# Performance work log

Hardware: AMD Instinct MI355X
Metric: run time of the kernel (lower is better)

The kernel has to match this reference:

```python
import jax, jax.numpy as jnp
import numpy as np

B, T, D, H, DH = 2, 1024, 1024, 16, 64
DFF, V = 4096, 32000
L0, NLAT, WIN = 512, 4, 3
R, ALPHA = 8, 16
LATENT_ID = 31999


def _ln(x, s, b):
    m = x.mean(-1, keepdims=True)
    v = ((x - m) ** 2).mean(-1, keepdims=True)
    return (x - m) * jax.lax.rsqrt(v + 1e-5) * s + b


def _lm(embeds, Wpos, Wqkv, bqkv, Aq, Bq, Wo, bo, Ao, Bo, W1, b1, W2, b2,
        ln1_s, ln1_b, ln2_s, ln2_b, lnf_s, lnf_b):
    # single pre-LN transformer block with LoRA-merged c_attn/c_proj + final LN
    S = embeds.shape[1]
    sc = ALPHA / R
    h = embeds + Wpos[:S]
    a = _ln(h, ln1_s, ln1_b)
    qkv = a @ (Wqkv + sc * (Aq @ Bq)) + bqkv          # [B,S,3D]
    q, k, v = [t.reshape(B, S, H, DH) for t in jnp.split(qkv, 3, axis=-1)]
    scores = jnp.einsum('bqhd,bkhd->bhqk', q, k) / 8.0  # sqrt(DH)=8
    mask = jnp.tril(jnp.ones((S, S), bool))
    attn = jax.nn.softmax(jnp.where(mask, scores, -1e9), axis=-1)
    ctx = jnp.einsum('bhqk,bkhd->bqhd', attn, v).reshape(B, S, D)
    h = h + ctx @ (Wo + sc * (Ao @ Bo)) + bo
    m = _ln(h, ln2_s, ln2_b)
    h = h + jax.nn.gelu(m @ W1 + b1) @ W2 + b2
    return _ln(h, lnf_s, lnf_b)


def setup_inputs() -> dict:
    key = jax.random.key(0)
    ks = jax.random.split(key, 16)
    init = lambda k, shape, scale: jax.random.normal(k, shape, jnp.float32) * scale
    input_ids = jax.random.randint(ks[0], (B, T), 0, V)
    input_ids = input_ids.at[:, L0:L0 + NLAT].set(LATENT_ID)  # latent slots
    return {
        'input_ids': input_ids.astype(jnp.int32),
        'attention_mask': jnp.ones((B, T), jnp.int32),
        'labels': jax.random.randint(ks[1], (B, T), 0, V).astype(jnp.int32),
        'position_ids': jnp.broadcast_to(jnp.arange(T, dtype=jnp.int32), (B, T)),
        'embed': init(ks[2], (V, D), 0.02),
        'Wpos': init(ks[3], (T, D), 0.01),
        'Wqkv': init(ks[4], (D, 3 * D), 0.02), 'bqkv': jnp.zeros((3 * D,)),
        'Aq': init(ks[5], (D, R), 0.02), 'Bq': init(ks[6], (R, 3 * D), 0.02),
        'Wo': init(ks[7], (D, D), 0.02), 'bo': jnp.zeros((D,)),
        'Ao': init(ks[8], (D, R), 0.02), 'Bo': init(ks[9], (R, D), 0.02),
        'W1': init(ks[10], (D, DFF), 0.02), 'b1': jnp.zeros((DFF,)),
        'W2': init(ks[11], (DFF, D), 0.02), 'b2': jnp.zeros((D,)),
        'ln1_s': jnp.ones((D,)), 'ln1_b': jnp.zeros((D,)),
        'ln2_s': jnp.ones((D,)), 'ln2_b': jnp.zeros((D,)),
        'lnf_s': jnp.ones((D,)), 'lnf_b': jnp.zeros((D,)),
        'latent_w': jnp.zeros((WIN,)),
    }


def reference(input_ids, attention_mask, labels, position_ids, embed, Wpos,
              Wqkv, bqkv, Aq, Bq, Wo, bo, Ao, Bo, W1, b1, W2, b2,
              ln1_s, ln1_b, ln2_s, ln2_b, lnf_s, lnf_b, latent_w):
    lm = lambda e: _lm(e, Wpos, Wqkv, bqkv, Aq, Bq, Wo, bo, Ao, Bo,
                       W1, b1, W2, b2, ln1_s, ln1_b, ln2_s, ln2_b, lnf_s, lnf_b)
    embeds = embed[input_ids]                     # [B,T,D]
    parts = []
    for p in range(NLAT):                         # fixed small iterative-pass count
        start = 0 if p == 0 else L0 + p - 1       # segment processed this pass
        end = L0 + p
        hid = lm(embeds[:, :end])                 # frozen-prefix recompute == kv cache
        parts.append(hid[:, start:end] @ embed.T) # segment logits (tied lm_head)
        tok = L0 + p                              # latent slot filled this pass
        n = min(WIN, tok - start)                 # window clipped to segment offset
        w = jax.nn.softmax(latent_w[WIN - n:])    # softmax over last n weights
        vec = jnp.einsum('w,bwd->bd', w, hid[:, tok - n:tok])
        embeds = embeds.at[:, tok].set(vec)       # scatter into latent slot
    hid = lm(embeds)
    parts.append(hid[:, L0 + NLAT - 1:] @ embed.T)
    logits = jnp.concatenate(parts, axis=1)       # [B,T,V]
    logp = jax.nn.log_softmax(logits[:, :-1], axis=-1)
    nll = -jnp.take_along_axis(logp, labels[:, 1:, None].astype(jnp.int32), axis=-1)
    return nll.mean()
```

## Files before the change

kernel.cpp:

```cpp
#include <hip/hip_runtime.h>
#include <math.h>

#define B_   2
#define T_   1024
#define D_   1024
#define H_   16
#define DH_  64
#define DFF_ 4096
#define V_   32000
#define NTOK 2046
#define NCH  250

typedef __attribute__((ext_vector_type(8))) short short8;
typedef __attribute__((ext_vector_type(4))) float floatx4;

__device__ __forceinline__ unsigned short f2bf(float x) {
    unsigned int u = __float_as_uint(x);
    unsigned int r = (u + 0x7fffu + ((u >> 16) & 1u)) >> 16;
    return (unsigned short)r;
}

__device__ __forceinline__ float bf2f(unsigned short u) {
    return __uint_as_float((unsigned int)u << 16);
}

__device__ __forceinline__ void gld_lds16(void* lds, const void* g) {
    __builtin_amdgcn_global_load_lds(
        (const __attribute__((address_space(1))) void*)g,
        (__attribute__((address_space(3))) void*)lds, 16, 0, 0);
}

__device__ __forceinline__ float gelu_tanh(float x) {
    float x3 = x * x * x;
    return 0.5f * x * (1.0f + tanhf(0.7978845608028654f * (x + 0.044715f * x3)));
}

__global__ __launch_bounds__(256) void k_prep_w(const float* __restrict__ W,
        const float* __restrict__ A, const float* __restrict__ Bm,
        unsigned short* __restrict__ out, int K, int N, int lora) {
    __shared__ float t[64][65];
    int n0 = blockIdx.x * 64, k0 = blockIdx.y * 64;
    int tid = threadIdx.x;
    int nn = tid & 63, kb = tid >> 6;
    for (int i = 0; i < 16; i++) {
        int kk = kb * 16 + i;
        float v = W[(size_t)(k0 + kk) * N + n0 + nn];
        if (lora) {
            float s = 0.f;
#pragma unroll
            for (int r = 0; r < 8; r++) s += A[(k0 + kk) * 8 + r] * Bm[r * N + n0 + nn];
            v += 2.0f * s;
        }
        t[kk][nn] = v;
    }
    __syncthreads();
    int kk2 = tid & 63, nb = tid >> 6;
    for (int j = 0; j < 16; j++) {
        int nn2 = nb * 16 + j;
        out[(size_t)(n0 + nn2) * K + k0 + kk2] = f2bf(t[kk2][nn2]);
    }
}

__global__ void k_f2bf(const float* __restrict__ in, unsigned short* __restrict__ out, int n4) {
    int i = blockIdx.x * 256 + threadIdx.x;
    if (i >= n4) return;
    float4 v = ((const float4*)in)[i];
    ushort4 o;
    o.x = f2bf(v.x); o.y = f2bf(v.y); o.z = f2bf(v.z); o.w = f2bf(v.w);
    ((ushort4*)out)[i] = o;
}

__global__ void k_embed_gather(const int* __restrict__ ids, const float* __restrict__ embed,
                               float* __restrict__ embeds) {
    int bt = blockIdx.x;
    int d4 = threadIdx.x;
    int id = ids[bt];
    ((float4*)embeds)[(size_t)bt * 256 + d4] = ((const float4*)embed)[(size_t)id * 256 + d4];
}

__global__ __launch_bounds__(256) void k_ln(const float* __restrict__ in,
                                            const float* __restrict__ embeds, const float* __restrict__ Wpos,
                                            const float* __restrict__ sc, const float* __restrict__ bi,
                                            float* __restrict__ hout, float* __restrict__ outf,
                                            unsigned short* __restrict__ outbf,
                                            int c0, int range, int strided_bf) {
    int r = blockIdx.x;
    int b = r / range, pos = c0 + r % range;
    size_t rowoff = (size_t)(b * T_ + pos) * D_;
    int tid = threadIdx.x;
    float xv[4];
    if (embeds) {
#pragma unroll
        for (int j = 0; j < 4; j++) {
            int i = tid + j * 256;
            xv[j] = embeds[rowoff + i] + Wpos[(size_t)pos * D_ + i];
            hout[rowoff + i] = xv[j];
        }
    } else {
#pragma unroll
        for (int j = 0; j < 4; j++) xv[j] = in[rowoff + tid + j * 256];
    }
    float s1 = 0.f, s2 = 0.f;
#pragma unroll
    for (int j = 0; j < 4; j++) { s1 += xv[j]; s2 += xv[j] * xv[j]; }
    __shared__ float r1[256], r2[256];
    r1[tid] = s1; r2[tid] = s2; __syncthreads();
    for (int o = 128; o > 0; o >>= 1) {
        if (tid < o) { r1[tid] += r1[tid + o]; r2[tid] += r2[tid + o]; }
        __syncthreads();
    }
    float mean = r1[0] * (1.0f / D_);
    float var = r2[0] * (1.0f / D_) - mean * mean;
    float inv = rsqrtf(var + 1e-5f);
    size_t bfrow = strided_bf ? (size_t)(b * T_ + pos) : (size_t)r;
#pragma unroll
    for (int j = 0; j < 4; j++) {
        int i = tid + j * 256;
        float y = (xv[j] - mean) * inv * sc[i] + bi[i];
        if (outf) outf[rowoff + i] = y;
        outbf[bfrow * D_ + i] = f2bf(y);
    }
}

template <int MODE>
__global__ __launch_bounds__(256) void k_mgemm(const unsigned short* __restrict__ Abf,
        const unsigned short* __restrict__ Bt, const float* __restrict__ bias,
        float* __restrict__ o0, unsigned short* __restrict__ u0,
        unsigned short* __restrict__ u1, unsigned short* __restrict__ u2,
        int M, int N, int K, int c0, int range, int ksegs) {
    __shared__ short8 As_v[256];
    __shared__ short8 Bs_v[512];
    int tid = threadIdx.x;
    int lane = tid & 63, w = tid >> 6;
    int quad = lane >> 4, l15 = lane & 15;
    int row0 = blockIdx.y * 64, col0 = blockIdx.x * 128;
    int kseg = blockIdx.z;
    int Klen = K / ksegs;
    int ksoff = kseg * Klen;
    int wr = w >> 1, wc = w & 1;

    int arow = row0 + lane; if (arow >= M) arow = M - 1;
    const unsigned short* ga  = Abf + (size_t)arow * K + ksoff + w * 8;
    int bcol = col0 + (w & 1) * 64 + lane;
    const unsigned short* gb1 = Bt + (size_t)bcol * K + ksoff + (w >> 1) * 8;
    const unsigned short* gb2 = Bt + (size_t)bcol * K + ksoff + (2 + (w >> 1)) * 8;

    floatx4 acc[2][4];
#pragma unroll
    for (int i = 0; i < 2; i++)
#pragma unroll
        for (int j = 0; j < 4; j++)
#pragma unroll
            for (int k = 0; k < 4; k++) acc[i][j][k] = 0.f;

    int iters = Klen >> 5;
    for (int it = 0; it < iters; ++it) {
        __syncthreads();
        gld_lds16(&As_v[w * 64],        ga);
        gld_lds16(&Bs_v[w * 64],        gb1);
        gld_lds16(&Bs_v[256 + w * 64],  gb2);
        ga += 32; gb1 += 32; gb2 += 32;
        __syncthreads();
        short8 af[2], bfv[4];
#pragma unroll
        for (int mi = 0; mi < 2; mi++) af[mi] = As_v[quad * 64 + wr * 32 + mi * 16 + l15];
#pragma unroll
        for (int nj = 0; nj < 4; nj++) bfv[nj] = Bs_v[quad * 128 + wc * 64 + nj * 16 + l15];
#pragma unroll
        for (int mi = 0; mi < 2; mi++)
#pragma unroll
            for (int nj = 0; nj < 4; nj++)
                acc[mi][nj] = __builtin_amdgcn_mfma_f32_16x16x32_bf16(af[mi], bfv[nj], acc[mi][nj], 0, 0, 0);
    }

#pragma unroll
    for (int mi = 0; mi < 2; mi++)
#pragma unroll
        for (int reg = 0; reg < 4; reg++) {
            int r = row0 + wr * 32 + mi * 16 + quad * 4 + reg;
            if (r >= M) continue;
            int b = r / range, pos = c0 + r % range;
#pragma unroll
            for (int nj = 0; nj < 4; nj++) {
                int n = col0 + wc * 64 + nj * 16 + l15;
                if constexpr (MODE == 1) {
                    float v = acc[mi][nj][reg] + bias[n];
                    if (n < 1024) u0[(size_t)r * 1024 + n] = f2bf(v);
                    else if (n < 2048) u1[(size_t)(b * T_ + pos) * 1024 + (n - 1024)] = f2bf(v);
                    else u2[(size_t)(b * T_ + pos) * 1024 + (n - 2048)] = f2bf(v);
                } else if constexpr (MODE == 2) {
                    float v = acc[mi][nj][reg] + (kseg == 0 ? bias[n] : 0.f);
                    atomicAdd(&o0[(size_t)(b * T_ + pos) * D_ + n], v);
                } else if constexpr (MODE == 3) {
                    float v = acc[mi][nj][reg] + bias[n];
                    u0[(size_t)r * N + n] = f2bf(gelu_tanh(v));
                }
            }
        }
}

template <int MODE>
__global__ __launch_bounds__(256) void k_sgemm(const unsigned short* __restrict__ Abf,
        const unsigned short* __restrict__ Bt, const float* __restrict__ bias,
        float* __restrict__ o0, unsigned short* __restrict__ u0,
        unsigned short* __restrict__ u1, unsigned short* __restrict__ u2,
        int N, int K, int c0) {
    __shared__ unsigned short lds_a[2 * 4096];
    __shared__ float lds_p[4][64][2];
    int tid = threadIdx.x, lane = tid & 63, w = tid >> 6;
    int n = blockIdx.x * 64 + lane;
    int nv = (2 * K) >> 3;
    for (int v = tid; v < nv; v += 256)
        *(short8*)&lds_a[v * 8] = *(const short8*)&Abf[v * 8];
    __syncthreads();
    int kq = K >> 2;
    int k0 = w * kq;
    float a0 = 0.f, a1 = 0.f;
    const unsigned short* bp = Bt + (size_t)n * K + k0;
    for (int i = 0; i < kq; i += 8) {
        short8 bv  = *(const short8*)(bp + i);
        short8 av0 = *(const short8*)&lds_a[k0 + i];
        short8 av1 = *(const short8*)&lds_a[K + k0 + i];
#pragma unroll
        for (int j = 0; j < 8; j++) {
            float bf_ = bf2f((unsigned short)bv[j]);
            a0 += bf2f((unsigned short)av0[j]) * bf_;
            a1 += bf2f((unsigned short)av1[j]) * bf_;
        }
    }
    lds_p[w][lane][0] = a0;
    lds_p[w][lane][1] = a1;
    __syncthreads();
    if (tid < 128) {
        int l = tid & 63, m = tid >> 6;
        int nn = blockIdx.x * 64 + l;
        float acc = lds_p[0][l][m] + lds_p[1][l][m] + lds_p[2][l][m] + lds_p[3][l][m];
        int b = m, pos = c0;
        if constexpr (MODE == 4) {
            float v = acc + bias[nn];
            if (nn < 1024) u0[(size_t)m * 1024 + nn] = f2bf(v);
            else if (nn < 2048) u1[(size_t)(b * T_ + pos) * 1024 + (nn - 1024)] = f2bf(v);
            else {
                int idx = nn - 2048, h = idx >> 6, d = idx & 63;
                u2[(size_t)((b * 16 + h) * 64 + d) * T_ + pos] = f2bf(v);
            }
        } else if constexpr (MODE == 2) {
            o0[(size_t)(b * T_ + pos) * D_ + nn] += acc + bias[nn];
        } else if constexpr (MODE == 3) {
            u0[(size_t)m * N + nn] = f2bf(gelu_tanh(acc + bias[nn]));
        }
    }
}

__global__ __launch_bounds__(256) void k_vtrans(const unsigned short* __restrict__ vcbf,
        unsigned short* __restrict__ vtc, int c0, int range) {
    __shared__ unsigned short ts[64][72];
    int pt = blockIdx.x, h = blockIdx.y, b = blockIdx.z;
    int t = threadIdx.x;
#pragma unroll
    for (int i = 0; i < 2; i++) {
        int idx = t + i * 256;
        int p = idx >> 3, c8 = idx & 7;
        int pos = c0 + pt * 64 + p;
        if (pos < c0 + range) {
            short8 v = *(const short8*)&vcbf[(size_t)(b * T_ + pos) * D_ + h * 64 + c8 * 8];
            *(short8*)&ts[p][c8 * 8] = v;
        }
    }
    __syncthreads();
#pragma unroll
    for (int i = 0; i < 2; i++) {
        int idx = t + i * 256;
        int d = idx >> 3, p8 = idx & 7;
        unsigned short tmp[8];
#pragma unroll
        for (int j = 0; j < 8; j++) tmp[j] = ts[p8 * 8 + j][d];
        int pos0 = c0 + pt * 64 + p8 * 8;
        size_t rb = (size_t)((b * 16 + h) * 64 + d) * T_;
        if (pos0 + 7 < c0 + range) {
            *(short8*)&vtc[rb + pos0] = *(short8*)tmp;
        } else {
            for (int j = 0; j < 8; j++)
                if (pos0 + j < c0 + range) vtc[rb + pos0 + j] = tmp[j];
        }
    }
}

__global__ __launch_bounds__(256) void k_fattn(const unsigned short* __restrict__ qbf,
        const unsigned short* __restrict__ kcbf, const unsigned short* __restrict__ vtc,
        unsigned short* __restrict__ ctxbf, int c0, int range) {
    __shared__ unsigned short pw[4][16][72];
    int tid = threadIdx.x;
    int w = tid >> 6, lane = tid & 63, quad = lane >> 4, l15 = lane & 15;
    int qt = blockIdx.x, h = blockIdx.y, b = blockIdx.z;
    int q0 = qt * 64 + w * 16;
    if (q0 >= range) return;
    int qtop = q0 + 15; if (qtop >= range) qtop = range - 1;
    int nkt = (c0 + qtop) / 64 + 1;

    int qrow = q0 + l15; if (qrow >= range) qrow = range - 1;
    const unsigned short* qp = qbf + (size_t)(b * range + qrow) * D_ + h * 64 + quad * 8;
    short8 aq0 = *(const short8*)qp;
    short8 aq1 = *(const short8*)(qp + 32);

    floatx4 oacc[4];
#pragma unroll
    for (int dg = 0; dg < 4; dg++)
#pragma unroll
        for (int r = 0; r < 4; r++) oacc[dg][r] = 0.f;
    float m_r[4] = {-1e30f, -1e30f, -1e30f, -1e30f};
    float l_r[4] = {0.f, 0.f, 0.f, 0.f};

    const unsigned short* kb_p = kcbf + (size_t)b * T_ * D_ + h * 64 + quad * 8;
    const unsigned short* vb_p = vtc + (size_t)((b * 16 + h) * 64 + l15) * T_ + quad * 8;

    for (int kt = 0; kt < nkt; kt++) {
        int kb = kt * 64;
        floatx4 s[4];
#pragma unroll
        for (int g = 0; g < 4; g++) {
            const unsigned short* kp = kb_p + (size_t)(kb + g * 16 + l15) * D_;
            short8 bk0 = *(const short8*)kp;
            short8 bk1 = *(const short8*)(kp + 32);
            floatx4 z; z[0] = 0.f; z[1] = 0.f; z[2] = 0.f; z[3] = 0.f;
            z = __builtin_amdgcn_mfma_f32_16x16x32_bf16(aq0, bk0, z, 0, 0, 0);
            s[g] = __builtin_amdgcn_mfma_f32_16x16x32_bf16(aq1, bk1, z, 0, 0, 0);
        }
#pragma unroll
        for (int r = 0; r < 4; r++) {
            int qpos = c0 + q0 + quad * 4 + r;
            float mx = -1e30f;
#pragma unroll
            for (int g = 0; g < 4; g++) {
                int kpos = kb + g * 16 + l15;
                float sv = (kpos <= qpos) ? s[g][r] * 0.125f : -1e30f;
                s[g][r] = sv; mx = fmaxf(mx, sv);
            }
            mx = fmaxf(mx, __shfl_xor(mx, 1));
            mx = fmaxf(mx, __shfl_xor(mx, 2));
            mx = fmaxf(mx, __shfl_xor(mx, 4));
            mx = fmaxf(mx, __shfl_xor(mx, 8));
            float mn = fmaxf(m_r[r], mx);
            float alpha = __expf(m_r[r] - mn);
            m_r[r] = mn;
            float ls = 0.f;
#pragma unroll
            for (int g = 0; g < 4; g++) {
                float p = __expf(s[g][r] - mn);
                s[g][r] = p; ls += p;
            }
            ls += __shfl_xor(ls, 1);
            ls += __shfl_xor(ls, 2);
            ls += __shfl_xor(ls, 4);
            ls += __shfl_xor(ls, 8);
            l_r[r] = l_r[r] * alpha + ls;
#pragma unroll
            for (int dg = 0; dg < 4; dg++) oacc[dg][r] *= alpha;
        }
#pragma unroll
        for (int g = 0; g < 4; g++)
#pragma unroll
            for (int r = 0; r < 4; r++)
                pw[w][quad * 4 + r][g * 16 + l15] = f2bf(s[g][r]);
        short8 ap0 = *(const short8*)&pw[w][l15][quad * 8];
        short8 ap1 = *(const short8*)&pw[w][l15][32 + quad * 8];
#pragma unroll
        for (int dg = 0; dg < 4; dg++) {
            const unsigned short* vp = vb_p + (size_t)(dg * 16) * T_ + kb;
            short8 bv0 = *(const short8*)vp;
            short8 bv1 = *(const short8*)(vp + 32);
            oacc[dg] = __builtin_amdgcn_mfma_f32_16x16x32_bf16(ap0, bv0, oacc[dg], 0, 0, 0);
            oacc[dg] = __builtin_amdgcn_mfma_f32_16x16x32_bf16(ap1, bv1, oacc[dg], 0, 0, 0);
        }
    }
#pragma unroll
    for (int dg = 0; dg < 4; dg++)
#pragma unroll
        for (int r = 0; r < 4; r++) {
            int qloc = q0 + quad * 4 + r;
            if (qloc < range)
                ctxbf[(size_t)(b * range + qloc) * D_ + h * 64 + dg * 16 + l15] =
                    f2bf(oacc[dg][r] / l_r[r]);
        }
}

__global__ void k_latent0(const float* __restrict__ hid, const float* __restrict__ lw,
                          float* __restrict__ embeds) {
    int idx = blockIdx.x * 256 + threadIdx.x;
    if (idx >= B_ * D_) return;
    int b = idx / D_, d = idx % D_;
    float w0 = lw[0], w1 = lw[1], w2 = lw[2];
    float mx = fmaxf(w0, fmaxf(w1, w2));
    float e0 = __expf(w0 - mx), e1 = __expf(w1 - mx), e2 = __expf(w2 - mx);
    float inv = 1.0f / (e0 + e1 + e2);
    float v = (e0 * hid[(size_t)(b * T_ + 509) * D_ + d] +
               e1 * hid[(size_t)(b * T_ + 510) * D_ + d] +
               e2 * hid[(size_t)(b * T_ + 511) * D_ + d]) * inv;
    embeds[(size_t)(b * T_ + 512) * D_ + d] = v;
}

__global__ void k_latent1(const float* __restrict__ hid, float* __restrict__ embeds, int tok) {
    int idx = blockIdx.x * 256 + threadIdx.x;
    if (idx >= B_ * D_) return;
    int b = idx / D_, d = idx % D_;
    embeds[(size_t)(b * T_ + tok) * D_ + d] = hid[(size_t)(b * T_ + tok - 1) * D_ + d];
}

__global__ __launch_bounds__(256) void k_loss1m(const unsigned short* __restrict__ hidbf,
        const unsigned short* __restrict__ embedbf, const int* __restrict__ labels,
        float* __restrict__ partm, float* __restrict__ parts, float* __restrict__ llogit) {
    __shared__ short8 As0[512], Bs0[512];
    __shared__ short8 As1[512], Bs1[512];
    __shared__ int lds_lab[128];
    __shared__ float lds_pm[128][2];
    __shared__ float lds_ps[128][2];
    int tid = threadIdx.x;
    int lane = tid & 63, w = tid >> 6;
    int quad = lane >> 4, l15 = lane & 15;
    int chunk = blockIdx.y;
    int row0 = blockIdx.x * 128, v0 = chunk * 128;
    int rh = (w >> 1) * 64, ch = (w & 1) * 64;

    if (tid < 128) {
        int tok = row0 + tid;
        lds_lab[tid] = (tok < NTOK) ? labels[tok + 1 + (tok >= 1023)] : -1;
    }

    int cA0 = w * 128 + lane, cA1 = cA0 + 64;
    int rA0 = cA0 & 127, kgA0 = cA0 >> 7;
    int rA1 = cA1 & 127, kgA1 = cA1 >> 7;
    int tokA0 = row0 + rA0; if (tokA0 >= NTOK) tokA0 = NTOK - 1;
    int tokA1 = row0 + rA1; if (tokA1 >= NTOK) tokA1 = NTOK - 1;
    const unsigned short* ga0 = hidbf + (size_t)(tokA0 + (tokA0 >= 1023)) * D_ + kgA0 * 8;
    const unsigned short* ga1 = hidbf + (size_t)(tokA1 + (tokA1 >= 1023)) * D_ + kgA1 * 8;
    const unsigned short* gb0 = embedbf + (size_t)(v0 + rA0) * D_ + kgA0 * 8;
    const unsigned short* gb1 = embedbf + (size_t)(v0 + rA1) * D_ + kgA1 * 8;

    floatx4 acc[4][4];
#pragma unroll
    for (int i = 0; i < 4; i++)
#pragma unroll
        for (int j = 0; j < 4; j++)
#pragma unroll
            for (int k = 0; k < 4; k++) acc[i][j][k] = 0.f;

#define LSTAGE(AS, BS) \
    gld_lds16(&AS[w * 128],      ga0); \
    gld_lds16(&AS[w * 128 + 64], ga1); \
    gld_lds16(&BS[w * 128],      gb0); \
    gld_lds16(&BS[w * 128 + 64], gb1); \
    ga0 += 32; ga1 += 32; gb0 += 32; gb1 += 32;

#define LCOMP(AS, BS) { \
    short8 af[4], bfv[4]; \
    _Pragma("unroll") \
    for (int mi = 0; mi < 4; mi++) af[mi] = AS[quad * 128 + rh + mi * 16 + l15]; \
    _Pragma("unroll") \
    for (int nj = 0; nj < 4; nj++) bfv[nj] = BS[quad * 128 + ch + nj * 16 + l15]; \
    _Pragma("unroll") \
    for (int mi = 0; mi < 4; mi++) \
        _Pragma("unroll") \
        for (int nj = 0; nj < 4; nj++) \
            acc[mi][nj] = __builtin_amdgcn_mfma_f32_16x16x32_bf16(af[mi], bfv[nj], acc[mi][nj], 0, 0, 0); }

#define WAIT_VM4_BAR \
    asm volatile("s_waitcnt vmcnt(4)" ::: "memory"); \
    __builtin_amdgcn_s_barrier(); \
    __builtin_amdgcn_sched_barrier(0);

#define WAIT_LGKM_BAR \
    asm volatile("s_waitcnt lgkmcnt(0)" ::: "memory"); \
    __builtin_amdgcn_s_barrier(); \
    __builtin_amdgcn_sched_barrier(0);

    LSTAGE(As0, Bs0)
    for (int itp = 0; itp < 15; ++itp) {
        LSTAGE(As1, Bs1)
        WAIT_VM4_BAR
        LCOMP(As0, Bs0)
        WAIT_LGKM_BAR
        LSTAGE(As0, Bs0)
        WAIT_VM4_BAR
        LCOMP(As1, Bs1)
        WAIT_LGKM_BAR
    }
    LSTAGE(As1, Bs1)
    WAIT_VM4_BAR
    LCOMP(As0, Bs0)
    WAIT_LGKM_BAR
    asm volatile("s_waitcnt vmcnt(0)" ::: "memory");
    __builtin_amdgcn_s_barrier();
    __builtin_amdgcn_sched_barrier(0);
    LCOMP(As1, Bs1)

#undef LSTAGE
#undef LCOMP
#undef WAIT_VM4_BAR
#undef WAIT_LGKM_BAR

#pragma unroll
    for (int mi = 0; mi < 4; mi++)
#pragma unroll
        for (int reg = 0; reg < 4; reg++) {
            int rloc = rh + mi * 16 + quad * 4 + reg;
            int lab = lds_lab[rloc];
            float vm = -1e30f;
#pragma unroll
            for (int nj = 0; nj < 4; nj++) {
                float v = acc[mi][nj][reg];
                int vcol = v0 + ch + nj * 16 + l15;
                if (vcol == lab) llogit[row0 + rloc] = v;
                vm = fmaxf(vm, v);
            }
            for (int off = 1; off < 16; off <<= 1) vm = fmaxf(vm, __shfl_xor(vm, off));
            float ss = 0.f;
#pragma unroll
            for (int nj = 0; nj < 4; nj++) ss += __expf(acc[mi][nj][reg] - vm);
            for (int off = 1; off < 16; off <<= 1) ss += __shfl_xor(ss, off);
            if (l15 == 0) { lds_pm[rloc][ch >> 6] = vm; lds_ps[rloc][ch >> 6] = ss; }
        }
    __syncthreads();
    if (tid < 128) {
        int tok = row0 + tid;
        if (tok < NTOK) {
            float m0 = lds_pm[tid][0], m1 = lds_pm[tid][1];
            float M = fmaxf(m0, m1);
            float S = lds_ps[tid][0] * __expf(m0 - M) + lds_ps[tid][1] * __expf(m1 - M);
            partm[(size_t)chunk * NTOK + tok] = M;
            parts[(size_t)chunk * NTOK + tok] = S;
        }
    }
}

__global__ void k_loss2a(const float* __restrict__ partm, const float* __restrict__ parts,
                         const float* __restrict__ ll, float* __restrict__ nll) {
    int tok = blockIdx.x * 256 + threadIdx.x;
    if (tok >= NTOK) return;
    float M = -1e30f;
    for (int c = 0; c < NCH; c++) M = fmaxf(M, partm[(size_t)c * NTOK + tok]);
    float S = 0.f;
    for (int c = 0; c < NCH; c++)
        S += parts[(size_t)c * NTOK + tok] * __expf(partm[(size_t)c * NTOK + tok] - M);
    nll[tok] = logf(S) + M - ll[tok];
}

__global__ __launch_bounds__(256) void k_loss2b(const float* __restrict__ nll, float* __restrict__ out) {
    __shared__ float red[256];
    int tid = threadIdx.x;
    float s = 0.f;
    for (int i = tid; i < NTOK; i += 256) s += nll[i];
    red[tid] = s; __syncthreads();
    for (int o = 128; o > 0; o >>= 1) {
        if (tid < o) red[tid] += red[tid + o];
        __syncthreads();
    }
    if (tid == 0) out[0] = red[0] / (float)NTOK;
}

extern "C" void kernel_launch(void* const* d_in, const int* in_sizes, int n_in,
                              void* d_out, int out_size, void* d_ws, size_t ws_size,
                              hipStream_t stream) {
    const int*   input_ids = (const int*)d_in[0];
    const int*   labels    = (const int*)d_in[2];
    const float* embed     = (const float*)d_in[4];
    const float* Wpos      = (const float*)d_in[5];
    const float* Wqkv      = (const float*)d_in[6];
    const float* bqkv      = (const float*)d_in[7];
    const float* Aq        = (const float*)d_in[8];
    const float* Bq        = (const float*)d_in[9];
    const float* Wo        = (const float*)d_in[10];
    const float* bo        = (const float*)d_in[11];
    const float* Ao        = (const float*)d_in[12];
    const float* Bo        = (const float*)d_in[13];
    const float* W1        = (const float*)d_in[14];
    const float* b1        = (const float*)d_in[15];
    const float* W2        = (const float*)d_in[16];
    const float* b2        = (const float*)d_in[17];
    const float* ln1_s     = (const float*)d_in[18];
    const float* ln1_b     = (const float*)d_in[19];
    const float* ln2_s     = (const float*)d_in[20];
    const float* ln2_b     = (const float*)d_in[21];
    const float* lnf_s     = (const float*)d_in[22];
    const float* lnf_b     = (const float*)d_in[23];
    const float* latent_w  = (const float*)d_in[24];

    char* base = (char*)d_ws;
    size_t off = 0;
    auto alloc = [&](size_t bytes) { void* p = base + off; off += (bytes + 255) & ~255ULL; return p; };

    float* embeds  = (float*)alloc((size_t)B_ * T_ * D_ * 4);
    float* hbuf    = (float*)alloc((size_t)B_ * T_ * D_ * 4);
    float* hidbuf  = (float*)alloc((size_t)B_ * T_ * D_ * 4);
    float* partm   = (float*)alloc((size_t)NCH * NTOK * 4);
    float* parts_  = (float*)alloc((size_t)NCH * NTOK * 4);
    float* llogit  = (float*)alloc((size_t)NTOK * 4);
    float* nllbuf  = (float*)alloc((size_t)NTOK * 4);
    unsigned short* wqkvT  = (unsigned short*)alloc((size_t)3072 * 1024 * 2);
    unsigned short* woT    = (unsigned short*)alloc((size_t)1024 * 1024 * 2);
    unsigned short* W1T    = (unsigned short*)alloc((size_t)4096 * 1024 * 2);
    unsigned short* W2T    = (unsigned short*)alloc((size_t)1024 * 4096 * 2);
    unsigned short* embedbf = (unsigned short*)alloc((size_t)V_ * D_ * 2);
    unsigned short* hidbf  = (unsigned short*)alloc((size_t)B_ * T_ * D_ * 2);
    unsigned short* abf    = (unsigned short*)alloc((size_t)1024 * D_ * 2);
    unsigned short* ctxbf  = (unsigned short*)alloc((size_t)1024 * D_ * 2);
    unsigned short* ffbw   = (unsigned short*)alloc((size_t)1024 * DFF_ * 2);
    unsigned short* qbf    = (unsigned short*)alloc((size_t)1024 * D_ * 2);
    unsigned short* kcbf   = (unsigned short*)alloc((size_t)B_ * T_ * D_ * 2);
    unsigned short* vcbf   = (unsigned short*)alloc((size_t)B_ * T_ * D_ * 2);
    unsigned short* vtc    = (unsigned short*)alloc((size_t)B_ * H_ * DH_ * T_ * 2);

    k_prep_w<<<dim3(3072 / 64, 1024 / 64), 256, 0, stream>>>(Wqkv, Aq, Bq, wqkvT, 1024, 3072, 1);
    k_prep_w<<<dim3(1024 / 64, 1024 / 64), 256, 0, stream>>>(Wo, Ao, Bo, woT, 1024, 1024, 1);
    k_prep_w<<<dim3(4096 / 64, 1024 / 64), 256, 0, stream>>>(W1, nullptr, nullptr, W1T, 1024, 4096, 0);
    k_prep_w<<<dim3(1024 / 64, 4096 / 64), 256, 0, stream>>>(W2, nullptr, nullptr, W2T, 4096, 1024, 0);
    k_f2bf<<<(V_ * D_ / 4 + 255) / 256, 256, 0, stream>>>(embed, embedbf, V_ * D_ / 4);
    k_embed_gather<<<B_ * T_, 256, 0, stream>>>(input_ids, embed, embeds);

    auto run_pass = [&](int c0, int c1) {
        int range = c1 - c0;
        int Mr = B_ * range;
        int gy = (Mr + 63) / 64;
        int qt = (range + 63) / 64;
        k_ln<<<Mr, 256, 0, stream>>>(nullptr, embeds, Wpos, ln1_s, ln1_b, hbuf, nullptr, abf, c0, range, 0);
        if (range == 1) {
            k_sgemm<4><<<3072 / 64, 256, 0, stream>>>(abf, wqkvT, bqkv, nullptr, qbf, kcbf, vtc,
                                                      3072, 1024, c0);
            k_fattn<<<dim3(1, H_, B_), 256, 0, stream>>>(qbf, kcbf, vtc, ctxbf, c0, 1);
            k_sgemm<2><<<1024 / 64, 256, 0, stream>>>(ctxbf, woT, bo, hbuf, nullptr, nullptr, nullptr,
                                                      1024, 1024, c0);
            k_ln<<<Mr, 256, 0, stream>>>(hbuf, nullptr, nullptr, ln2_s, ln2_b, nullptr, nullptr, abf, c0, range, 0);
            k_sgemm<3><<<4096 / 64, 256, 0, stream>>>(abf, W1T, b1, nullptr, ffbw, nullptr, nullptr,
                                                      4096, 1024, c0);
            k_sgemm<2><<<1024 / 64, 256, 0, stream>>>(ffbw, W2T, b2, hbuf, nullptr, nullptr, nullptr,
                                                      1024, 4096, c0);
        } else {
            k_mgemm<1><<<dim3(3072 / 128, gy), 256, 0, stream>>>(abf, wqkvT, bqkv, nullptr, qbf, kcbf, vcbf,
                                                                 Mr, 3072, 1024, c0, range, 1);
            k_vtrans<<<dim3(qt, H_, B_), 256, 0, stream>>>(vcbf, vtc, c0, range);
            k_fattn<<<dim3(qt, H_, B_), 256, 0, stream>>>(qbf, kcbf, vtc, ctxbf, c0, range);
            k_mgemm<2><<<dim3(1024 / 128, gy, 4), 256, 0, stream>>>(ctxbf, woT, bo, hbuf, nullptr, nullptr, nullptr,
                                                                    Mr, 1024, 1024, c0, range, 4);
            k_ln<<<Mr, 256, 0, stream>>>(hbuf, nullptr, nullptr, ln2_s, ln2_b, nullptr, nullptr, abf, c0, range, 0);
            k_mgemm<3><<<dim3(4096 / 128, gy), 256, 0, stream>>>(abf, W1T, b1, nullptr, ffbw, nullptr, nullptr,
                                                                 Mr, 4096, 1024, c0, range, 1);
            k_mgemm<2><<<dim3(1024 / 128, gy, 4), 256, 0, stream>>>(ffbw, W2T, b2, hbuf, nullptr, nullptr, nullptr,
                                                                    Mr, 1024, 4096, c0, range, 4);
        }
        k_ln<<<Mr, 256, 0, stream>>>(hbuf, nullptr, nullptr, lnf_s, lnf_b, nullptr, hidbuf, hidbf, c0, range, 1);
    };

    run_pass(0, 512);
    k_latent0<<<(B_ * D_ + 255) / 256, 256, 0, stream>>>(hidbuf, latent_w, embeds);
    run_pass(512, 513);
    k_latent1<<<(B_ * D_ + 255) / 256, 256, 0, stream>>>(hidbuf, embeds, 513);
    run_pass(513, 514);
    k_latent1<<<(B_ * D_ + 255) / 256, 256, 0, stream>>>(hidbuf, embeds, 514);
    run_pass(514, 515);
    k_latent1<<<(B_ * D_ + 255) / 256, 256, 0, stream>>>(hidbuf, embeds, 515);
    run_pass(515, 1024);

    k_loss1m<<<dim3((NTOK + 127) / 128, NCH), 256, 0, stream>>>(hidbf, embedbf, labels, partm, parts_, llogit);
    k_loss2a<<<(NTOK + 255) / 256, 256, 0, stream>>>(partm, parts_, llogit, nllbuf);
    k_loss2b<<<1, 256, 0, stream>>>(nllbuf, (float*)d_out);
}
```

Measured before the change: 1.264 ms.

## Double-buffer MFMA GEMM LDS loads and split-K the single-token GEMV kernels

The tiled MFMA GEMM now keeps two LDS buffers and issues the next K-tile's global-to-LDS loads before computing the current tile, using vmcnt waits and raw barriers so load latency overlaps the MFMA work. The single-row (range==1) GEMV path is split along K into more blocks, with partial sums either written to a scratch buffer and reduced by a finish kernel or accumulated with atomics, to use more CUs. This costs double the LDS per block, extra kernel launches and atomics, and the pipelined loop assumes an even number of K iterations.

```diff
diff --git a/kernel.cpp b/kernel.cpp
--- a/kernel.cpp
+++ b/kernel.cpp
@@ -128,8 +128,8 @@
         float* __restrict__ o0, unsigned short* __restrict__ u0,
         unsigned short* __restrict__ u1, unsigned short* __restrict__ u2,
         int M, int N, int K, int c0, int range, int ksegs) {
-    __shared__ short8 As_v[256];
-    __shared__ short8 Bs_v[512];
+    __shared__ short8 As0[256], Bs0[512];
+    __shared__ short8 As1[256], Bs1[512];
     int tid = threadIdx.x;
     int lane = tid & 63, w = tid >> 6;
     int quad = lane >> 4, l15 = lane & 15;
@@ -154,24 +154,50 @@
             for (int k = 0; k < 4; k++) acc[i][j][k] = 0.f;
 
     int iters = Klen >> 5;
-    for (int it = 0; it < iters; ++it) {
-        __syncthreads();
-        gld_lds16(&As_v[w * 64],        ga);
-        gld_lds16(&Bs_v[w * 64],        gb1);
-        gld_lds16(&Bs_v[256 + w * 64],  gb2);
-        ga += 32; gb1 += 32; gb2 += 32;
-        __syncthreads();
-        short8 af[2], bfv[4];
-#pragma unroll
-        for (int mi = 0; mi < 2; mi++) af[mi] = As_v[quad * 64 + wr * 32 + mi * 16 + l15];
-#pragma unroll
-        for (int nj = 0; nj < 4; nj++) bfv[nj] = Bs_v[quad * 128 + wc * 64 + nj * 16 + l15];
-#pragma unroll
-        for (int mi = 0; mi < 2; mi++)
-#pragma unroll
-            for (int nj = 0; nj < 4; nj++)
-                acc[mi][nj] = __builtin_amdgcn_mfma_f32_16x16x32_bf16(af[mi], bfv[nj], acc[mi][nj], 0, 0, 0);
-    }
+
+#define MSTAGE(AS, BS) \
+    gld_lds16(&AS[w * 64],       ga); \
+    gld_lds16(&BS[w * 64],       gb1); \
+    gld_lds16(&BS[256 + w * 64], gb2); \
+    ga += 32; gb1 += 32; gb2 += 32;
+
+#define MCOMP(AS, BS) { \
+    short8 af[2], bfv[4]; \
+    _Pragma("unroll") \
+    for (int mi = 0; mi < 2; mi++) af[mi] = AS[quad * 64 + wr * 32 + mi * 16 + l15]; \
+    _Pragma("unroll") \
+    for (int nj = 0; nj < 4; nj++) bfv[nj] = BS[quad * 128 + wc * 64 + nj * 16 + l15]; \
+    _Pragma("unroll") \
+    for (int mi = 0; mi < 2; mi++) \
+        _Pragma("unroll") \
+        for (int nj = 0; nj < 4; nj++) \
+            acc[mi][nj] = __builtin_amdgcn_mfma_f32_16x16x32_bf16(af[mi], bfv[nj], acc[mi][nj], 0, 0, 0); }
+
+#define MWVM3 \
+    asm volatile("s_waitcnt vmcnt(3)" ::: "memory"); \
+    __builtin_amdgcn_s_barrier(); \
+    __builtin_amdgcn_sched_barrier(0);
+
+#define MWLG \
+    asm volatile("s_waitcnt lgkmcnt(0)" ::: "memory"); \
+    __builtin_amdgcn_s_barrier(); \
+    __builtin_amdgcn_sched_barrier(0);
+
+    MSTAGE(As0, Bs0)
+    for (int itp = 0; itp < (iters >> 1) - 1; ++itp) {
+        MSTAGE(As1, Bs1) MWVM3 MCOMP(As0, Bs0) MWLG
+        MSTAGE(As0, Bs0) MWVM3 MCOMP(As1, Bs1) MWLG
+    }
+    MSTAGE(As1, Bs1) MWVM3 MCOMP(As0, Bs0) MWLG
+    asm volatile("s_waitcnt vmcnt(0)" ::: "memory");
+    __builtin_amdgcn_s_barrier();
+    __builtin_amdgcn_sched_barrier(0);
+    MCOMP(As1, Bs1)
+
+#undef MSTAGE
+#undef MCOMP
+#undef MWVM3
+#undef MWLG
 
 #pragma unroll
     for (int mi = 0; mi < 2; mi++)
@@ -199,28 +225,26 @@
         }
 }
 
-template <int MODE>
-__global__ __launch_bounds__(256) void k_sgemm(const unsigned short* __restrict__ Abf,
-        const unsigned short* __restrict__ Bt, const float* __restrict__ bias,
-        float* __restrict__ o0, unsigned short* __restrict__ u0,
-        unsigned short* __restrict__ u1, unsigned short* __restrict__ u2,
-        int N, int K, int c0) {
-    __shared__ unsigned short lds_a[2 * 4096];
+__global__ __launch_bounds__(256) void k_sp_part(const unsigned short* __restrict__ Abf,
+        const unsigned short* __restrict__ Bt, float* __restrict__ pacc, int N, int K) {
+    __shared__ unsigned short lds_a[2][256];
     __shared__ float lds_p[4][64][2];
     int tid = threadIdx.x, lane = tid & 63, w = tid >> 6;
     int n = blockIdx.x * 64 + lane;
-    int nv = (2 * K) >> 3;
-    for (int v = tid; v < nv; v += 256)
-        *(short8*)&lds_a[v * 8] = *(const short8*)&Abf[v * 8];
+    int kseg = blockIdx.y, k0 = kseg * 256;
+    if (tid < 64) {
+        int m = tid >> 5, j = tid & 31;
+        *(short8*)&lds_a[m][j * 8] = *(const short8*)&Abf[(size_t)m * K + k0 + j * 8];
+    }
     __syncthreads();
-    int kq = K >> 2;
-    int k0 = w * kq;
+    int kw = w * 64;
     float a0 = 0.f, a1 = 0.f;
-    const unsigned short* bp = Bt + (size_t)n * K + k0;
-    for (int i = 0; i < kq; i += 8) {
+    const unsigned short* bp = Bt + (size_t)n * K + k0 + kw;
+#pragma unroll
+    for (int i = 0; i < 64; i += 8) {
         short8 bv  = *(const short8*)(bp + i);
-        short8 av0 = *(const short8*)&lds_a[k0 + i];
-        short8 av1 = *(const short8*)&lds_a[K + k0 + i];
+        short8 av0 = *(const short8*)&lds_a[0][kw + i];
+        short8 av1 = *(const short8*)&lds_a[1][kw + i];
 #pragma unroll
         for (int j = 0; j < 8; j++) {
             float bf_ = bf2f((unsigned short)bv[j]);
@@ -235,20 +259,69 @@
         int l = tid & 63, m = tid >> 6;
         int nn = blockIdx.x * 64 + l;
         float acc = lds_p[0][l][m] + lds_p[1][l][m] + lds_p[2][l][m] + lds_p[3][l][m];
-        int b = m, pos = c0;
-        if constexpr (MODE == 4) {
-            float v = acc + bias[nn];
-            if (nn < 1024) u0[(size_t)m * 1024 + nn] = f2bf(v);
-            else if (nn < 2048) u1[(size_t)(b * T_ + pos) * 1024 + (nn - 1024)] = f2bf(v);
-            else {
-                int idx = nn - 2048, h = idx >> 6, d = idx & 63;
-                u2[(size_t)((b * 16 + h) * 64 + d) * T_ + pos] = f2bf(v);
-            }
-        } else if constexpr (MODE == 2) {
-            o0[(size_t)(b * T_ + pos) * D_ + nn] += acc + bias[nn];
-        } else if constexpr (MODE == 3) {
-            u0[(size_t)m * N + nn] = f2bf(gelu_tanh(acc + bias[nn]));
-        }
+        pacc[((size_t)kseg * 2 + m) * N + nn] = acc;
+    }
+}
+
+__global__ __launch_bounds__(256) void k_sp_add(const unsigned short* __restrict__ Abf,
+        const unsigned short* __restrict__ Bt, const float* __restrict__ bias,
+        float* __restrict__ o0, int N, int K, int c0) {
+    __shared__ unsigned short lds_a[2][256];
+    __shared__ float lds_p[4][64][2];
+    int tid = threadIdx.x, lane = tid & 63, w = tid >> 6;
+    int n = blockIdx.x * 64 + lane;
+    int kseg = blockIdx.y, k0 = kseg * 256;
+    if (tid < 64) {
+        int m = tid >> 5, j = tid & 31;
+        *(short8*)&lds_a[m][j * 8] = *(const short8*)&Abf[(size_t)m * K + k0 + j * 8];
+    }
+    __syncthreads();
+    int kw = w * 64;
+    float a0 = 0.f, a1 = 0.f;
+    const unsigned short* bp = Bt + (size_t)n * K + k0 + kw;
+#pragma unroll
+    for (int i = 0; i < 64; i += 8) {
+        short8 bv  = *(const short8*)(bp + i);
+        short8 av0 = *(const short8*)&lds_a[0][kw + i];
+        short8 av1 = *(const short8*)&lds_a[1][kw + i];
+#pragma unroll
+        for (int j = 0; j < 8; j++) {
+            float bf_ = bf2f((unsigned short)bv[j]);
+            a0 += bf2f((unsigned short)av0[j]) * bf_;
+            a1 += bf2f((unsigned short)av1[j]) * bf_;
+        }
+    }
+    lds_p[w][lane][0] = a0;
+    lds_p[w][lane][1] = a1;
+    __syncthreads();
+    if (tid < 128) {
+        int l = tid & 63, m = tid >> 6;
+        int nn = blockIdx.x * 64 + l;
+        float acc = lds_p[0][l][m] + lds_p[1][l][m] + lds_p[2][l][m] + lds_p[3][l][m];
+        if (kseg == 0) acc += bias[nn];
+        atomicAdd(&o0[(size_t)(m * T_ + c0) * D_ + nn], acc);
+    }
+}
+
+template <int MODE>
+__global__ void k_sp_fin(const float* __restrict__ pacc, const float* __restrict__ bias,
+        unsigned short* __restrict__ u0, unsigned short* __restrict__ u1,
+        unsigned short* __restrict__ u2, int N, int nseg, int c0) {
+    int idx = blockIdx.x * 256 + threadIdx.x;
+    if (idx >= 2 * N) return;
+    int m = idx / N, n = idx % N;
+    float s = 0.f;
+    for (int k = 0; k < nseg; k++) s += pacc[((size_t)k * 2 + m) * N + n];
+    s += bias[n];
+    if constexpr (MODE == 4) {
+        if (n < 1024) u0[(size_t)m * 1024 + n] = f2bf(s);
+        else if (n < 2048) u1[(size_t)(m * T_ + c0) * 1024 + (n - 1024)] = f2bf(s);
+        else {
+            int id2 = n - 2048, h = id2 >> 6, d = id2 & 63;
+            u2[(size_t)((m * 16 + h) * 64 + d) * T_ + c0] = f2bf(s);
+        }
+    } else {
+        u0[(size_t)m * N + n] = f2bf(gelu_tanh(s));
     }
 }
 
@@ -595,6 +668,7 @@
     float* parts_  = (float*)alloc((size_t)NCH * NTOK * 4);
     float* llogit  = (float*)alloc((size_t)NTOK * 4);
     float* nllbuf  = (float*)alloc((size_t)NTOK * 4);
+    float* pacc    = (float*)alloc((size_t)16 * 2 * 4096 * 4);
     unsigned short* wqkvT  = (unsigned short*)alloc((size_t)3072 * 1024 * 2);
     unsigned short* woT    = (unsigned short*)alloc((size_t)1024 * 1024 * 2);
     unsigned short* W1T    = (unsigned short*)alloc((size_t)4096 * 1024 * 2);
@@ -623,16 +697,14 @@
         int qt = (range + 63) / 64;
         k_ln<<<Mr, 256, 0, stream>>>(nullptr, embeds, Wpos, ln1_s, ln1_b, hbuf, nullptr, abf, c0, range, 0);
         if (range == 1) {
-            k_sgemm<4><<<3072 / 64, 256, 0, stream>>>(abf, wqkvT, bqkv, nullptr, qbf, kcbf, vtc,
-                                                      3072, 1024, c0);
+            k_sp_part<<<dim3(48, 4), 256, 0, stream>>>(abf, wqkvT, pacc, 3072, 1024);
+            k_sp_fin<4><<<24, 256, 0, stream>>>(pacc, bqkv, qbf, kcbf, vtc, 3072, 4, c0);
             k_fattn<<<dim3(1, H_, B_), 256, 0, stream>>>(qbf, kcbf, vtc, ctxbf, c0, 1);
-            k_sgemm<2><<<1024 / 64, 256, 0, stream>>>(ctxbf, woT, bo, hbuf, nullptr, nullptr, nullptr,
-                                                      1024, 1024, c0);
+            k_sp_add<<<dim3(16, 4), 256, 0, stream>>>(ctxbf, woT, bo, hbuf, 1024, 1024, c0);
             k_ln<<<Mr, 256, 0, stream>>>(hbuf, nullptr, nullptr, ln2_s, ln2_b, nullptr, nullptr, abf, c0, range, 0);
-            k_sgemm<3><<<4096 / 64, 256, 0, stream>>>(abf, W1T, b1, nullptr, ffbw, nullptr, nullptr,
-                                                      4096, 1024, c0);
-            k_sgemm<2><<<1024 / 64, 256, 0, stream>>>(ffbw, W2T, b2, hbuf, nullptr, nullptr, nullptr,
-                                                      1024, 4096, c0);
+            k_sp_part<<<dim3(64, 4), 256, 0, stream>>>(abf, W1T, pacc, 4096, 1024);
+            k_sp_fin<3><<<32, 256, 0, stream>>>(pacc, b1, ffbw, nullptr, nullptr, 4096, 4, c0);
+            k_sp_add<<<dim3(16, 16), 256, 0, stream>>>(ffbw, W2T, b2, hbuf, 1024, 4096, c0);
         } else {
             k_mgemm<1><<<dim3(3072 / 128, gy), 256, 0, stream>>>(abf, wqkvT, bqkv, nullptr, qbf, kcbf, vcbf,
                                                                  Mr, 3072, 1024, c0, range, 1);
```

Result: faster. 1.173 ms (-7.2%).
